# Performance work log

Hardware: AMD Instinct MI355X
Metric: run time of the kernel (lower is better)

Reference implementation:

```python
import jax, jax.numpy as jnp
import numpy as np

N, C, H, W = 16, 512, 32, 32
OC = C // 8  # shrink = 8


def setup_inputs() -> dict:
    key = jax.random.key(0)
    ks = jax.random.split(key, 8)
    s = lambda fan: 1.0 / np.sqrt(fan)
    return {
        "tensor": jax.random.normal(ks[0], (N, C, H, W), dtype=jnp.float32),
        "key_w": jax.random.normal(ks[1], (OC, C), dtype=jnp.float32) * s(C),
        "key_b": jax.random.normal(ks[2], (OC,), dtype=jnp.float32) * 0.01,
        "query_w": jax.random.normal(ks[3], (OC, C), dtype=jnp.float32) * s(C),
        "query_b": jax.random.normal(ks[4], (OC,), dtype=jnp.float32) * 0.01,
        "value_w": jax.random.normal(ks[5], (C, C), dtype=jnp.float32) * s(C),
        "value_b": jax.random.normal(ks[6], (C,), dtype=jnp.float32) * 0.01,
        "gamma": jax.random.normal(ks[7], (1,), dtype=jnp.float32),
    }


def reference(tensor, key_w, key_b, query_w, query_b, value_w, value_b, gamma):
    n, c, h, w = tensor.shape
    x = tensor.reshape(n, c, h * w)  # [n, c, hw]
    # 1x1 convs are per-position linear maps over channels
    k = jnp.einsum("oc,ncp->nop", key_w, x) + key_b[None, :, None]      # [n, oc, hw]
    q = jnp.einsum("oc,ncp->nop", query_w, x) + query_b[None, :, None]  # [n, oc, hw]
    v = jnp.einsum("oc,ncp->nop", value_w, x) + value_b[None, :, None]  # [n, c, hw]
    # unscaled attention: softmax over keys (last dim)
    scores = jnp.einsum("ncq,nck->nqk", q, k)  # [n, hw, hw]
    attn = jax.nn.softmax(scores, axis=2)
    o = jnp.einsum("nck,nqk->ncq", v, attn).reshape(n, c, h, w)
    return tensor + o * gamma[0]
```

## Files before the change

### kernel.cpp

```cpp
#include <hip/hip_runtime.h>
#include <hip/hip_bf16.h>

typedef __hip_bfloat16 bf16;
typedef __attribute__((ext_vector_type(8))) short bf16x8;
typedef __attribute__((ext_vector_type(4))) float f32x4;

#define NBATCH 16
#define CCH    512
#define PP     1024
#define OCH    64

__device__ __forceinline__ void gload16(const void* g, void* l) {
  __builtin_amdgcn_global_load_lds(
      (const __attribute__((address_space(1))) void*)g,
      (__attribute__((address_space(3))) void*)l, 16, 0, 0);
}
__device__ __forceinline__ float bf2f(bf16 v) { return __bfloat162float(v); }
__device__ __forceinline__ bf16  f2bf(float v) { return __float2bfloat16(v); }

__device__ __forceinline__ void barrier_vm0() {
  asm volatile("s_waitcnt vmcnt(0)" ::: "memory");
  __builtin_amdgcn_s_barrier();
  asm volatile("" ::: "memory");
}
__device__ __forceinline__ void barrier_lgkm0() {
  asm volatile("s_waitcnt lgkmcnt(0)" ::: "memory");
  __builtin_amdgcn_s_barrier();
  asm volatile("" ::: "memory");
}

__global__ __launch_bounds__(256) void prep_transpose_kernel(
    const float* __restrict__ x,
    const float* __restrict__ key_w, const float* __restrict__ key_b,
    const float* __restrict__ query_w, const float* __restrict__ query_b,
    const float* __restrict__ value_w, const float* __restrict__ value_b,
    bf16* __restrict__ xhi, bf16* __restrict__ xlo,
    bf16* __restrict__ wqk_hi, bf16* __restrict__ wqk_lo,
    bf16* __restrict__ wv, float* __restrict__ bias_qk, float* __restrict__ bias_v) {
  __shared__ float tile[64 * 65];
  const int bid = blockIdx.x;
  const int tid = threadIdx.x;
  if (bid < 2048) {
    const int pt = bid & 15, ct = (bid >> 4) & 7, n = bid >> 7;
    const size_t xbase = ((size_t)n * CCH + ct * 64) * PP + pt * 64;
#pragma unroll
    for (int i = 0; i < 4; ++i) {
      const int chunk = i * 256 + tid;
      const int row = chunk >> 4, c4 = chunk & 15;
      const f32x4 v = *(const f32x4*)&x[xbase + (size_t)row * PP + c4 * 4];
#pragma unroll
      for (int m = 0; m < 4; ++m) tile[row * 65 + c4 * 4 + m] = v[m];
    }
    __syncthreads();
    const size_t obase = ((size_t)n * PP + pt * 64) * CCH + ct * 64;
#pragma unroll
    for (int ii = 0; ii < 2; ++ii) {
      const int p = ii * 32 + (tid >> 3);
      const int cu = tid & 7;
      bf16x8 hv, lv;
#pragma unroll
      for (int j = 0; j < 8; ++j) {
        const float f = tile[(cu * 8 + j) * 65 + p];
        const bf16 h = f2bf(f);
        const bf16 lo_ = f2bf(f - bf2f(h));
        short hs, ls;
        __builtin_memcpy(&hs, &h, 2);
        __builtin_memcpy(&ls, &lo_, 2);
        hv[j] = hs;
        lv[j] = ls;
      }
      const size_t oidx = obase + (size_t)p * CCH + cu * 8;
      *(bf16x8*)&xhi[oidx] = hv;
      *(bf16x8*)&xlo[oidx] = lv;
    }
  } else {
    const int t = (bid - 2048) * 256 + tid;
    const int TOT_QK = 128 * 512;
    const int TOT_V  = 512 * 512;
    if (t < TOT_QK) {
      const int m = t >> 9, c = t & 511;
      const float v = (m < 64) ? query_w[m * 512 + c] : key_w[(m - 64) * 512 + c];
      const bf16 hi = f2bf(v);
      wqk_hi[t] = hi;
      wqk_lo[t] = f2bf(v - bf2f(hi));
    } else if (t < TOT_QK + TOT_V) {
      const int u = t - TOT_QK;
      wv[u] = f2bf(value_w[u]);
    } else if (t < TOT_QK + TOT_V + 128) {
      const int m = t - (TOT_QK + TOT_V);
      bias_qk[m] = (m < 64) ? query_b[m] : key_b[m - 64];
    } else if (t < TOT_QK + TOT_V + 128 + 512) {
      const int m = t - (TOT_QK + TOT_V + 128);
      bias_v[m] = value_b[m];
    }
  }
}

__global__ __launch_bounds__(256) void gemm_qkv_kernel(
    const bf16* __restrict__ Whi, const bf16* __restrict__ Wlo,
    const bf16* __restrict__ Wv,
    const bf16* __restrict__ XThi, const bf16* __restrict__ XTlo,
    const float* __restrict__ biasqk, const float* __restrict__ biasv,
    bf16* __restrict__ qhi, bf16* __restrict__ qlo,
    bf16* __restrict__ khi, bf16* __restrict__ klo,
    bf16* __restrict__ Vout) {
  __shared__ __align__(16) bf16 sm[4 * 128 * 64];
  const int tid = threadIdx.x, l = tid & 63, w = tid >> 6;
  const int lrow = l >> 3, lcol = (l & 7) * 8, wr = w >> 1, wc = w & 1;
  const f32x4 z = {0.f, 0.f, 0.f, 0.f};
  f32x4 acc[4][4];
#pragma unroll
  for (int i = 0; i < 4; ++i)
#pragma unroll
    for (int j = 0; j < 4; ++j) acc[i][j] = z;

  if (blockIdx.x < 128) {
    const int id = blockIdx.x;
    const int n0 = (id & 7) * 128, bn = id >> 3;
    const size_t xoff = (size_t)bn * PP * CCH;
    bf16* Ash = sm;
    bf16* Asl = sm + 8192;
    bf16* Bsh = sm + 16384;
    bf16* Bsl = sm + 24576;
    for (int kt = 0; kt < CCH; kt += 64) {
#pragma unroll
      for (int it = 0; it < 4; ++it) {
        const int chunk = w * 4 + it;
        const int ar = chunk * 8 + lrow;
        const int br = n0 + chunk * 8 + lrow;
        gload16(Whi + (size_t)ar * CCH + kt + lcol, &Ash[chunk * 512]);
        gload16(Wlo + (size_t)ar * CCH + kt + lcol, &Asl[chunk * 512]);
        gload16(XThi + xoff + (size_t)br * CCH + kt + lcol, &Bsh[chunk * 512]);
        gload16(XTlo + xoff + (size_t)br * CCH + kt + lcol, &Bsl[chunk * 512]);
      }
      __syncthreads();
#pragma unroll
      for (int kk = 0; kk < 2; ++kk) {
        bf16x8 ah[4], al[4], bh[4], bl[4];
        const int ko = kk * 32 + (l >> 4) * 8;
#pragma unroll
        for (int i = 0; i < 4; ++i) {
          const int r = (wr * 64 + i * 16 + (l & 15)) * 64 + ko;
          ah[i] = *(const bf16x8*)&Ash[r];
          al[i] = *(const bf16x8*)&Asl[r];
        }
#pragma unroll
        for (int j = 0; j < 4; ++j) {
          const int r = (wc * 64 + j * 16 + (l & 15)) * 64 + ko;
          bh[j] = *(const bf16x8*)&Bsh[r];
          bl[j] = *(const bf16x8*)&Bsl[r];
        }
#pragma unroll
        for (int i = 0; i < 4; ++i)
#pragma unroll
          for (int j = 0; j < 4; ++j) {
            acc[i][j] = __builtin_amdgcn_mfma_f32_16x16x32_bf16(ah[i], bh[j], acc[i][j], 0, 0, 0);
            acc[i][j] = __builtin_amdgcn_mfma_f32_16x16x32_bf16(ah[i], bl[j], acc[i][j], 0, 0, 0);
            acc[i][j] = __builtin_amdgcn_mfma_f32_16x16x32_bf16(al[i], bh[j], acc[i][j], 0, 0, 0);
          }
      }
      __syncthreads();
    }
    const size_t qoff = (size_t)bn * PP * OCH;
#pragma unroll
    for (int i = 0; i < 4; ++i)
#pragma unroll
      for (int j = 0; j < 4; ++j)
#pragma unroll
        for (int r = 0; r < 4; ++r) {
          const int m = wr * 64 + i * 16 + (l >> 4) * 4 + r;
          const int p = n0 + wc * 64 + j * 16 + (l & 15);
          const float v = acc[i][j][r] + biasqk[m];
          const bf16 hi = f2bf(v);
          const bf16 lo = f2bf(v - bf2f(hi));
          if (m < 64) {
            qhi[qoff + (size_t)p * OCH + m] = hi;
            qlo[qoff + (size_t)p * OCH + m] = lo;
          } else {
            khi[qoff + (size_t)p * OCH + (m - 64)] = hi;
            klo[qoff + (size_t)p * OCH + (m - 64)] = lo;
          }
        }
  } else {
    const int id = blockIdx.x - 128;
    const int n0 = (id & 7) * 128, m0 = ((id >> 3) & 3) * 128, bn = id >> 5;
    const size_t xoff = (size_t)bn * PP * CCH;
    bf16* As = sm;
    bf16* Bs = sm + 8192;
    for (int kt = 0; kt < CCH; kt += 64) {
#pragma unroll
      for (int it = 0; it < 4; ++it) {
        const int chunk = w * 4 + it;
        gload16(Wv + (size_t)(m0 + chunk * 8 + lrow) * CCH + kt + lcol, &As[chunk * 512]);
        gload16(XThi + xoff + (size_t)(n0 + chunk * 8 + lrow) * CCH + kt + lcol, &Bs[chunk * 512]);
      }
      __syncthreads();
#pragma unroll
      for (int kk = 0; kk < 2; ++kk) {
        bf16x8 a[4], b[4];
        const int ko = kk * 32 + (l >> 4) * 8;
#pragma unroll
        for (int i = 0; i < 4; ++i) a[i] = *(const bf16x8*)&As[(wr * 64 + i * 16 + (l & 15)) * 64 + ko];
#pragma unroll
        for (int j = 0; j < 4; ++j) b[j] = *(const bf16x8*)&Bs[(wc * 64 + j * 16 + (l & 15)) * 64 + ko];
#pragma unroll
        for (int i = 0; i < 4; ++i)
#pragma unroll
          for (int j = 0; j < 4; ++j)
            acc[i][j] = __builtin_amdgcn_mfma_f32_16x16x32_bf16(a[i], b[j], acc[i][j], 0, 0, 0);
      }
      __syncthreads();
    }
#pragma unroll
    for (int i = 0; i < 4; ++i)
#pragma unroll
      for (int j = 0; j < 4; ++j)
#pragma unroll
        for (int r = 0; r < 4; ++r) {
          const int m = m0 + wr * 64 + i * 16 + (l >> 4) * 4 + r;
          const int p = n0 + wc * 64 + j * 16 + (l & 15);
          Vout[(size_t)bn * CCH * PP + (size_t)m * PP + p] = f2bf(acc[i][j][r] + biasv[m]);
        }
  }
}

#define KT 32
#define NT 32

__global__ __launch_bounds__(512, 2) void fused_attn_kernel(
    const bf16* __restrict__ qhi, const bf16* __restrict__ qlo,
    const bf16* __restrict__ khi, const bf16* __restrict__ klo,
    const bf16* __restrict__ vbuf, const float* __restrict__ tensor,
    const float* __restrict__ gamma, float* __restrict__ out) {
  __shared__ __align__(16) char smem[102400];
  __shared__ float red[128];
  __shared__ float fq[64];
  const int tid = threadIdx.x, l = tid & 63, w = tid >> 6;

  const int d = blockIdx.x;
  const int idx = d >> 3;
  const int bn = (d & 7) * 2 + (idx >> 4);
  const int qt0 = (idx & 15) * 64;

  const size_t qkoff = (size_t)bn * PP * OCH;
  const size_t voff  = (size_t)bn * CCH * PP;
  char* Qh = smem;
  char* Ql = smem + 8192;
  char* Pb = smem + 98304;

  {
    const int s = (w << 6) | l;
    const int row = s >> 3, pu = s & 7, lu = pu ^ (row & 7);
    const size_t src = qkoff + (size_t)(qt0 + row) * OCH + lu * 8;
    gload16(qhi + src, Qh + w * 1024);
    gload16(qlo + src, Ql + w * 1024);
  }
  barrier_vm0();

  bf16x8 ah[2], al[2];
  {
    const int qrow = ((w & 3) << 4) + (l & 15);
#pragma unroll
    for (int h = 0; h < 2; ++h) {
      const int lu = (l >> 4) + 4 * h, pu = lu ^ (qrow & 7);
      ah[h] = *(const bf16x8*)(Qh + qrow * 128 + pu * 16);
      al[h] = *(const bf16x8*)(Ql + qrow * 128 + pu * 16);
    }
  }

  auto stage_kv = [&](int t, char* khD, char* klD, char* vD) {
    {
      const int s = ((w & 3) << 6) | l;
      const int row = s >> 3, pu = s & 7, lu = pu ^ (row & 7);
      const bf16* srcp = ((w < 4) ? khi : klo) + qkoff + (size_t)(t * KT + row) * OCH + lu * 8;
      gload16(srcp, ((w < 4) ? khD : klD) + (w & 3) * 1024);
    }
#pragma unroll
    for (int c4 = 0; c4 < 4; ++c4) {
      const int s = (w << 8) + (c4 << 6) + l;
      const int row = s >> 2, pu = s & 3, lu = pu ^ ((row >> 1) & 3);
      const bf16* srcp = vbuf + voff + (size_t)row * PP + t * KT + lu * 8;
      gload16(srcp, vD + ((w << 8) + (c4 << 6)) * 16);
    }
  };

  stage_kv(0, smem + 16384, smem + 24576, smem + 32768);

  f32x4 acc[4][4];
  const f32x4 z = {0.f, 0.f, 0.f, 0.f};
#pragma unroll
  for (int i = 0; i < 4; ++i)
#pragma unroll
    for (int j = 0; j < 4; ++j) acc[i][j] = z;
  float psum[4] = {0.f, 0.f, 0.f, 0.f};
  const int kf = w >> 2;

  for (int t = 0; t < NT; ++t) {
    char* khB = smem + 16384 + ((t & 1) ? 4096 : 0);
    char* klB = smem + 24576 + ((t & 1) ? 4096 : 0);
    char* vB  = smem + 32768 + ((t & 1) ? 32768 : 0);

    barrier_vm0();

    if (t + 1 < NT) {
      stage_kv(t + 1,
               smem + 16384 + ((t & 1) ? 0 : 4096),
               smem + 24576 + ((t & 1) ? 0 : 4096),
               smem + 32768 + ((t & 1) ? 0 : 32768));
    }

    bf16x8 kh_[2], kl_[2];
    const int krow = (kf << 4) + (l & 15);
#pragma unroll
    for (int h = 0; h < 2; ++h) {
      const int lu = (l >> 4) + 4 * h, pu = lu ^ (krow & 7);
      kh_[h] = *(const bf16x8*)(khB + krow * 128 + pu * 16);
      kl_[h] = *(const bf16x8*)(klB + krow * 128 + pu * 16);
    }
    __builtin_amdgcn_s_setprio(1);
    f32x4 s = z;
    s = __builtin_amdgcn_mfma_f32_16x16x32_bf16(ah[0], kh_[0], s, 0, 0, 0);
    s = __builtin_amdgcn_mfma_f32_16x16x32_bf16(ah[1], kh_[1], s, 0, 0, 0);
    s = __builtin_amdgcn_mfma_f32_16x16x32_bf16(al[0], kh_[0], s, 0, 0, 0);
    s = __builtin_amdgcn_mfma_f32_16x16x32_bf16(al[1], kh_[1], s, 0, 0, 0);
    s = __builtin_amdgcn_mfma_f32_16x16x32_bf16(ah[0], kl_[0], s, 0, 0, 0);
    s = __builtin_amdgcn_mfma_f32_16x16x32_bf16(ah[1], kl_[1], s, 0, 0, 0);
    __builtin_amdgcn_s_setprio(0);

#pragma unroll
    for (int r = 0; r < 4; ++r) {
      const float pv = __expf(s[r] - 30.f);
      const bf16 pb16 = f2bf(pv);
      psum[r] += bf2f(pb16);
      const int q = ((w & 3) << 4) + ((l >> 4) << 2) + r;
      const int k = (kf << 4) + (l & 15);
      const int pu = (k >> 3) ^ ((q >> 1) & 3);
      *(bf16*)(Pb + q * 64 + pu * 16 + (k & 7) * 2) = pb16;
    }
    barrier_lgkm0();

    bf16x8 va[4], pb[4];
#pragma unroll
    for (int i = 0; i < 4; ++i) {
      const int crow = (w << 6) + (i << 4) + (l & 15);
      const int pu = (l >> 4) ^ ((crow >> 1) & 3);
      va[i] = *(const bf16x8*)(vB + crow * 64 + pu * 16);
    }
#pragma unroll
    for (int j = 0; j < 4; ++j) {
      const int prow = (j << 4) + (l & 15);
      const int pu = (l >> 4) ^ ((prow >> 1) & 3);
      pb[j] = *(const bf16x8*)(Pb + prow * 64 + pu * 16);
    }
    __builtin_amdgcn_s_setprio(1);
#pragma unroll
    for (int i = 0; i < 4; ++i)
#pragma unroll
      for (int j = 0; j < 4; ++j)
        acc[i][j] = __builtin_amdgcn_mfma_f32_16x16x32_bf16(va[i], pb[j], acc[i][j], 0, 0, 0);
    __builtin_amdgcn_s_setprio(0);
  }

#pragma unroll
  for (int off = 1; off < 16; off <<= 1)
#pragma unroll
    for (int r = 0; r < 4; ++r) psum[r] += __shfl_xor(psum[r], off);
  if ((l & 15) == 0) {
#pragma unroll
    for (int r = 0; r < 4; ++r) {
      const int q = ((w & 3) << 4) + ((l >> 4) << 2) + r;
      red[q * 2 + kf] = psum[r];
    }
  }
  __syncthreads();
  if (tid < 64) fq[tid] = gamma[0] / (red[tid * 2] + red[tid * 2 + 1]);
  __syncthreads();

  float* rep = (float*)smem;
  for (int half = 0; half < 2; ++half) {
    if ((w >> 2) == half) {
#pragma unroll
      for (int i = 0; i < 4; ++i)
#pragma unroll
        for (int j = 0; j < 4; ++j) {
          const int q = (j << 4) + (l & 15);
          const float f = fq[q];
          const int c0 = ((w & 3) << 6) + (i << 4) + ((l >> 4) << 2);
#pragma unroll
          for (int r = 0; r < 4; ++r) rep[(c0 + r) * 68 + q] = acc[i][j][r] * f;
        }
    }
    __syncthreads();
#pragma unroll
    for (int it = 0; it < 8; ++it) {
      const int chunk = it * 512 + tid;
      const int cl = chunk >> 4, ch = chunk & 15;
      const size_t gi = ((size_t)bn * CCH + half * 256 + cl) * PP + qt0 + ch * 4;
      const f32x4 tv = *(const f32x4*)&tensor[gi];
      const f32x4 rv = *(const f32x4*)&rep[cl * 68 + ch * 4];
      *(f32x4*)&out[gi] = tv + rv;
    }
    __syncthreads();
  }
}

extern "C" void kernel_launch(void* const* d_in, const int* in_sizes, int n_in,
                              void* d_out, int out_size, void* d_ws, size_t ws_size,
                              hipStream_t stream) {
  const float* tensor  = (const float*)d_in[0];
  const float* key_w   = (const float*)d_in[1];
  const float* key_b   = (const float*)d_in[2];
  const float* query_w = (const float*)d_in[3];
  const float* query_b = (const float*)d_in[4];
  const float* value_w = (const float*)d_in[5];
  const float* value_b = (const float*)d_in[6];
  const float* gamma   = (const float*)d_in[7];

  char* ws = (char*)d_ws;
  size_t off = 0;
  auto alloc = [&](size_t bytes) -> char* {
    char* p = ws + off;
    off += (bytes + 255) & ~(size_t)255;
    return p;
  };
  bf16* xt_hi  = (bf16*)alloc((size_t)NBATCH * PP * CCH * 2);
  bf16* xt_lo  = (bf16*)alloc((size_t)NBATCH * PP * CCH * 2);
  bf16* wqk_hi = (bf16*)alloc(128 * 512 * 2);
  bf16* wqk_lo = (bf16*)alloc(128 * 512 * 2);
  bf16* wv     = (bf16*)alloc(512 * 512 * 2);
  float* bias_qk = (float*)alloc(128 * 4);
  float* bias_v  = (float*)alloc(512 * 4);
  bf16* q_hi = (bf16*)alloc((size_t)NBATCH * PP * OCH * 2);
  bf16* q_lo = (bf16*)alloc((size_t)NBATCH * PP * OCH * 2);
  bf16* k_hi = (bf16*)alloc((size_t)NBATCH * PP * OCH * 2);
  bf16* k_lo = (bf16*)alloc((size_t)NBATCH * PP * OCH * 2);
  bf16* vbuf = (bf16*)alloc((size_t)NBATCH * CCH * PP * 2);
  (void)ws_size; (void)in_sizes; (void)n_in; (void)out_size;

  prep_transpose_kernel<<<dim3(3331), dim3(256), 0, stream>>>(
      tensor, key_w, key_b, query_w, query_b, value_w, value_b,
      xt_hi, xt_lo, wqk_hi, wqk_lo, wv, bias_qk, bias_v);

  gemm_qkv_kernel<<<dim3(640), dim3(256), 0, stream>>>(
      wqk_hi, wqk_lo, wv, xt_hi, xt_lo, bias_qk, bias_v,
      q_hi, q_lo, k_hi, k_lo, vbuf);

  fused_attn_kernel<<<dim3(256), dim3(512), 0, stream>>>(
      q_hi, q_lo, k_hi, k_lo, vbuf, tensor, gamma, (float*)d_out);
}
```

Baseline: 96.56 us.

## Software-pipeline PV matmul one tile behind QK scores with double-buffered P

Restructures the fused attention loop so the P·V MFMA for tile t-1 is issued in the same iteration as the QK^T score MFMAs for tile t. The P buffer is double-buffered in LDS, which grows shared memory by 4 KB, and the epilogue drains the last PV step. The aim is to overlap the exp/softmax write phase with matrix work and to remove the mid-iteration dependency stall. In exchange it adds a second barrier per iteration, more LDS use that may affect the 2-blocks-per-CU occupancy, and extra live registers for va/pb.

```diff
diff --git a/kernel.cpp b/kernel.cpp
--- a/kernel.cpp
+++ b/kernel.cpp
@@ -17,17 +17,6 @@
 }
 __device__ __forceinline__ float bf2f(bf16 v) { return __bfloat162float(v); }
 __device__ __forceinline__ bf16  f2bf(float v) { return __float2bfloat16(v); }
-
-__device__ __forceinline__ void barrier_vm0() {
-  asm volatile("s_waitcnt vmcnt(0)" ::: "memory");
-  __builtin_amdgcn_s_barrier();
-  asm volatile("" ::: "memory");
-}
-__device__ __forceinline__ void barrier_lgkm0() {
-  asm volatile("s_waitcnt lgkmcnt(0)" ::: "memory");
-  __builtin_amdgcn_s_barrier();
-  asm volatile("" ::: "memory");
-}
 
 __global__ __launch_bounds__(256) void prep_transpose_kernel(
     const float* __restrict__ x,
@@ -232,7 +221,7 @@
     const bf16* __restrict__ khi, const bf16* __restrict__ klo,
     const bf16* __restrict__ vbuf, const float* __restrict__ tensor,
     const float* __restrict__ gamma, float* __restrict__ out) {
-  __shared__ __align__(16) char smem[102400];
+  __shared__ __align__(16) char smem[106496];
   __shared__ float red[128];
   __shared__ float fq[64];
   const int tid = threadIdx.x, l = tid & 63, w = tid >> 6;
@@ -246,7 +235,6 @@
   const size_t voff  = (size_t)bn * CCH * PP;
   char* Qh = smem;
   char* Ql = smem + 8192;
-  char* Pb = smem + 98304;
 
   {
     const int s = (w << 6) | l;
@@ -255,7 +243,9 @@
     gload16(qhi + src, Qh + w * 1024);
     gload16(qlo + src, Ql + w * 1024);
   }
-  barrier_vm0();
+  asm volatile("s_waitcnt vmcnt(0)" ::: "memory");
+  __builtin_amdgcn_s_barrier();
+  asm volatile("" ::: "memory");
 
   bf16x8 ah[2], al[2];
   {
@@ -295,18 +285,43 @@
   float psum[4] = {0.f, 0.f, 0.f, 0.f};
   const int kf = w >> 2;
 
+  bf16x8 va[4], pb[4];
+
   for (int t = 0; t < NT; ++t) {
-    char* khB = smem + 16384 + ((t & 1) ? 4096 : 0);
-    char* klB = smem + 24576 + ((t & 1) ? 4096 : 0);
-    char* vB  = smem + 32768 + ((t & 1) ? 32768 : 0);
-
-    barrier_vm0();
+    const int buf = t & 1, pbuf = (t + 1) & 1;
+    char* khB = smem + 16384 + buf * 4096;
+    char* klB = smem + 24576 + buf * 4096;
+    char* PbC = smem + 98304 + buf * 4096;
+
+    asm volatile("s_waitcnt vmcnt(0) lgkmcnt(0)" ::: "memory");
+    __builtin_amdgcn_s_barrier();
+    asm volatile("" ::: "memory");
+
+    if (t > 0) {
+      char* vP = smem + 32768 + pbuf * 32768;
+      char* PbP = smem + 98304 + pbuf * 4096;
+#pragma unroll
+      for (int i = 0; i < 4; ++i) {
+        const int crow = (w << 6) + (i << 4) + (l & 15);
+        const int pu = (l >> 4) ^ ((crow >> 1) & 3);
+        va[i] = *(const bf16x8*)(vP + crow * 64 + pu * 16);
+      }
+#pragma unroll
+      for (int j = 0; j < 4; ++j) {
+        const int prow = (j << 4) + (l & 15);
+        const int pu = (l >> 4) ^ ((prow >> 1) & 3);
+        pb[j] = *(const bf16x8*)(PbP + prow * 64 + pu * 16);
+      }
+    }
+    asm volatile("s_waitcnt lgkmcnt(0)" ::: "memory");
+    __builtin_amdgcn_s_barrier();
+    asm volatile("" ::: "memory");
 
     if (t + 1 < NT) {
       stage_kv(t + 1,
-               smem + 16384 + ((t & 1) ? 0 : 4096),
-               smem + 24576 + ((t & 1) ? 0 : 4096),
-               smem + 32768 + ((t & 1) ? 0 : 32768));
+               smem + 16384 + (buf ? 0 : 4096),
+               smem + 24576 + (buf ? 0 : 4096),
+               smem + 32768 + (buf ? 0 : 32768));
     }
 
     bf16x8 kh_[2], kl_[2];
@@ -317,7 +332,15 @@
       kh_[h] = *(const bf16x8*)(khB + krow * 128 + pu * 16);
       kl_[h] = *(const bf16x8*)(klB + krow * 128 + pu * 16);
     }
+
     __builtin_amdgcn_s_setprio(1);
+    if (t > 0) {
+#pragma unroll
+      for (int i = 0; i < 4; ++i)
+#pragma unroll
+        for (int j = 0; j < 4; ++j)
+          acc[i][j] = __builtin_amdgcn_mfma_f32_16x16x32_bf16(va[i], pb[j], acc[i][j], 0, 0, 0);
+    }
     f32x4 s = z;
     s = __builtin_amdgcn_mfma_f32_16x16x32_bf16(ah[0], kh_[0], s, 0, 0, 0);
     s = __builtin_amdgcn_mfma_f32_16x16x32_bf16(ah[1], kh_[1], s, 0, 0, 0);
@@ -335,30 +358,34 @@
       const int q = ((w & 3) << 4) + ((l >> 4) << 2) + r;
       const int k = (kf << 4) + (l & 15);
       const int pu = (k >> 3) ^ ((q >> 1) & 3);
-      *(bf16*)(Pb + q * 64 + pu * 16 + (k & 7) * 2) = pb16;
-    }
-    barrier_lgkm0();
-
-    bf16x8 va[4], pb[4];
+      *(bf16*)(PbC + q * 64 + pu * 16 + (k & 7) * 2) = pb16;
+    }
+  }
+
+  asm volatile("s_waitcnt lgkmcnt(0)" ::: "memory");
+  __builtin_amdgcn_s_barrier();
+  asm volatile("" ::: "memory");
+  {
+    const int pbuf = (NT - 1) & 1;
+    char* vP = smem + 32768 + pbuf * 32768;
+    char* PbP = smem + 98304 + pbuf * 4096;
 #pragma unroll
     for (int i = 0; i < 4; ++i) {
       const int crow = (w << 6) + (i << 4) + (l & 15);
       const int pu = (l >> 4) ^ ((crow >> 1) & 3);
-      va[i] = *(const bf16x8*)(vB + crow * 64 + pu * 16);
+      va[i] = *(const bf16x8*)(vP + crow * 64 + pu * 16);
     }
 #pragma unroll
     for (int j = 0; j < 4; ++j) {
       const int prow = (j << 4) + (l & 15);
       const int pu = (l >> 4) ^ ((prow >> 1) & 3);
-      pb[j] = *(const bf16x8*)(Pb + prow * 64 + pu * 16);
-    }
-    __builtin_amdgcn_s_setprio(1);
+      pb[j] = *(const bf16x8*)(PbP + prow * 64 + pu * 16);
+    }
 #pragma unroll
     for (int i = 0; i < 4; ++i)
 #pragma unroll
       for (int j = 0; j < 4; ++j)
         acc[i][j] = __builtin_amdgcn_mfma_f32_16x16x32_bf16(va[i], pb[j], acc[i][j], 0, 0, 0);
-    __builtin_amdgcn_s_setprio(0);
   }
 
 #pragma unroll
```

New measurement: 99.26 us. +2.8%, slower.

## Single-buffer V tile and shrink LDS to raise attention kernel occupancy

Applied to the files above, without the earlier changes.

V staging becomes single-buffered: the next V tile is loaded only after the PV MFMAs finish, behind an extra barrier. K stays double-buffered. This cuts the fused attention kernel's LDS from about 100KB to 68KB, and the launch bound rises to four 512-thread blocks per CU. The epilogue now writes the output in four 128-channel chunks so the reduction buffer fits in the smaller LDS. In exchange, V loads no longer overlap with compute, and the tighter register budget may force the 64-float accumulator to spill.

```diff
diff --git a/kernel.cpp b/kernel.cpp
--- a/kernel.cpp
+++ b/kernel.cpp
@@ -25,6 +25,11 @@
 }
 __device__ __forceinline__ void barrier_lgkm0() {
   asm volatile("s_waitcnt lgkmcnt(0)" ::: "memory");
+  __builtin_amdgcn_s_barrier();
+  asm volatile("" ::: "memory");
+}
+__device__ __forceinline__ void barrier_plain() {
+  asm volatile("" ::: "memory");
   __builtin_amdgcn_s_barrier();
   asm volatile("" ::: "memory");
 }
@@ -227,12 +232,12 @@
 #define KT 32
 #define NT 32
 
-__global__ __launch_bounds__(512, 2) void fused_attn_kernel(
+__global__ __launch_bounds__(512, 4) void fused_attn_kernel(
     const bf16* __restrict__ qhi, const bf16* __restrict__ qlo,
     const bf16* __restrict__ khi, const bf16* __restrict__ klo,
     const bf16* __restrict__ vbuf, const float* __restrict__ tensor,
     const float* __restrict__ gamma, float* __restrict__ out) {
-  __shared__ __align__(16) char smem[102400];
+  __shared__ __align__(16) char smem[69632];
   __shared__ float red[128];
   __shared__ float fq[64];
   const int tid = threadIdx.x, l = tid & 63, w = tid >> 6;
@@ -246,7 +251,8 @@
   const size_t voff  = (size_t)bn * CCH * PP;
   char* Qh = smem;
   char* Ql = smem + 8192;
-  char* Pb = smem + 98304;
+  char* Vb = smem + 32768;
+  char* Pb = smem + 65536;
 
   {
     const int s = (w << 6) | l;
@@ -255,6 +261,27 @@
     gload16(qhi + src, Qh + w * 1024);
     gload16(qlo + src, Ql + w * 1024);
   }
+
+  auto stage_k = [&](int t, int buf) {
+    char* base = smem + 16384 + ((w >= 4) ? 8192 : 0) + buf * 4096;
+    const bf16* src0 = (w < 4) ? khi : klo;
+    const int s = ((w & 3) << 6) | l;
+    const int row = s >> 3, pu = s & 7, lu = pu ^ (row & 7);
+    gload16(src0 + qkoff + (size_t)(t * KT + row) * OCH + lu * 8,
+            base + (w & 3) * 1024);
+  };
+  auto stage_v = [&](int t) {
+#pragma unroll
+    for (int c4 = 0; c4 < 4; ++c4) {
+      const int s = (w << 8) + (c4 << 6) + l;
+      const int row = s >> 2, pu = s & 3, lu = pu ^ ((row >> 1) & 3);
+      const bf16* srcp = vbuf + voff + (size_t)row * PP + t * KT + lu * 8;
+      gload16(srcp, Vb + ((w << 8) + (c4 << 6)) * 16);
+    }
+  };
+
+  stage_k(0, 0);
+  stage_v(0);
   barrier_vm0();
 
   bf16x8 ah[2], al[2];
@@ -268,24 +295,6 @@
     }
   }
 
-  auto stage_kv = [&](int t, char* khD, char* klD, char* vD) {
-    {
-      const int s = ((w & 3) << 6) | l;
-      const int row = s >> 3, pu = s & 7, lu = pu ^ (row & 7);
-      const bf16* srcp = ((w < 4) ? khi : klo) + qkoff + (size_t)(t * KT + row) * OCH + lu * 8;
-      gload16(srcp, ((w < 4) ? khD : klD) + (w & 3) * 1024);
-    }
-#pragma unroll
-    for (int c4 = 0; c4 < 4; ++c4) {
-      const int s = (w << 8) + (c4 << 6) + l;
-      const int row = s >> 2, pu = s & 3, lu = pu ^ ((row >> 1) & 3);
-      const bf16* srcp = vbuf + voff + (size_t)row * PP + t * KT + lu * 8;
-      gload16(srcp, vD + ((w << 8) + (c4 << 6)) * 16);
-    }
-  };
-
-  stage_kv(0, smem + 16384, smem + 24576, smem + 32768);
-
   f32x4 acc[4][4];
   const f32x4 z = {0.f, 0.f, 0.f, 0.f};
 #pragma unroll
@@ -296,19 +305,13 @@
   const int kf = w >> 2;
 
   for (int t = 0; t < NT; ++t) {
-    char* khB = smem + 16384 + ((t & 1) ? 4096 : 0);
-    char* klB = smem + 24576 + ((t & 1) ? 4096 : 0);
-    char* vB  = smem + 32768 + ((t & 1) ? 32768 : 0);
-
-    barrier_vm0();
-
-    if (t + 1 < NT) {
-      stage_kv(t + 1,
-               smem + 16384 + ((t & 1) ? 0 : 4096),
-               smem + 24576 + ((t & 1) ? 0 : 4096),
-               smem + 32768 + ((t & 1) ? 0 : 32768));
-    }
-
+    const int buf = t & 1;
+    if (t) barrier_vm0();
+
+    if (t + 1 < NT) stage_k(t + 1, buf ^ 1);
+
+    char* khB = smem + 16384 + buf * 4096;
+    char* klB = smem + 24576 + buf * 4096;
     bf16x8 kh_[2], kl_[2];
     const int krow = (kf << 4) + (l & 15);
 #pragma unroll
@@ -344,7 +347,7 @@
     for (int i = 0; i < 4; ++i) {
       const int crow = (w << 6) + (i << 4) + (l & 15);
       const int pu = (l >> 4) ^ ((crow >> 1) & 3);
-      va[i] = *(const bf16x8*)(vB + crow * 64 + pu * 16);
+      va[i] = *(const bf16x8*)(Vb + crow * 64 + pu * 16);
     }
 #pragma unroll
     for (int j = 0; j < 4; ++j) {
@@ -359,6 +362,9 @@
       for (int j = 0; j < 4; ++j)
         acc[i][j] = __builtin_amdgcn_mfma_f32_16x16x32_bf16(va[i], pb[j], acc[i][j], 0, 0, 0);
     __builtin_amdgcn_s_setprio(0);
+
+    barrier_plain();
+    if (t + 1 < NT) stage_v(t + 1);
   }
 
 #pragma unroll
@@ -377,27 +383,28 @@
   __syncthreads();
 
   float* rep = (float*)smem;
-  for (int half = 0; half < 2; ++half) {
-    if ((w >> 2) == half) {
+  const size_t obase = (size_t)bn * CCH * PP + qt0;
+#pragma unroll
+  for (int chunk = 0; chunk < 4; ++chunk) {
+    if ((w >> 1) == chunk) {
 #pragma unroll
       for (int i = 0; i < 4; ++i)
 #pragma unroll
         for (int j = 0; j < 4; ++j) {
           const int q = (j << 4) + (l & 15);
           const float f = fq[q];
-          const int c0 = ((w & 3) << 6) + (i << 4) + ((l >> 4) << 2);
+          const int c0 = ((w & 1) << 6) + (i << 4) + ((l >> 4) << 2);
 #pragma unroll
           for (int r = 0; r < 4; ++r) rep[(c0 + r) * 68 + q] = acc[i][j][r] * f;
         }
     }
     __syncthreads();
 #pragma unroll
-    for (int it = 0; it < 8; ++it) {
-      const int chunk = it * 512 + tid;
-      const int cl = chunk >> 4, ch = chunk & 15;
-      const size_t gi = ((size_t)bn * CCH + half * 256 + cl) * PP + qt0 + ch * 4;
+    for (int it = 0; it < 4; ++it) {
+      const int cp = it * 512 + tid, cl = cp >> 4, q4 = cp & 15;
+      const size_t gi = obase + (size_t)(chunk * 128 + cl) * PP + q4 * 4;
       const f32x4 tv = *(const f32x4*)&tensor[gi];
-      const f32x4 rv = *(const f32x4*)&rep[cl * 68 + ch * 4];
+      const f32x4 rv = *(const f32x4*)&rep[cl * 68 + q4 * 4];
       *(f32x4*)&out[gi] = tv + rv;
     }
     __syncthreads();
```

Measured after the change: 153.2 us. +58.6%, slower.
